# Performance work log

Measured on AMD Instinct MI355X. Metric: run time of the kernel, lower is better.

The kernel has to match this reference:

```python
import jax, jax.numpy as jnp
import numpy as np

SECURE_MIN = 1e-5
EPS = 1e-20
N_ITER = 10

def _l1_normalize(t, axis):
    # F.normalize(p=1): t / max(||t||_1, eps); t is nonnegative here so |t| = t
    n = jnp.sum(jnp.abs(t), axis=axis, keepdims=True)
    return t / jnp.maximum(n, EPS)

def setup_inputs() -> dict:
    key = jax.random.key(0)
    kx, kw = jax.random.split(key)
    B, F_in, F_out = 2048, 4096, 2048
    x = jax.random.uniform(kx, (B, F_in), dtype=jnp.float32)
    W = jax.random.uniform(kw, (F_out, F_in), dtype=jnp.float32)
    return {"x": x, "W": W}

def reference(x, W):
    B = x.shape[0]
    F_out = W.shape[0]
    # normalize_weights: clamp to secure min, L1-normalize each row (over input dim)
    Wn = _l1_normalize(jnp.clip(W, SECURE_MIN), axis=1)  # (F_out, F_in)
    # _prepare_input: L1 normalize over feature dim
    xn = _l1_normalize(x, axis=-1)  # (B, F_in)
    # _reset_h: uniform h over output units
    h0 = jnp.full((B, F_out), 1.0 / F_out, dtype=x.dtype)

    def step(h, _):
        # _reconstruct: h @ W -> input space
        recon = h @ Wn                                   # (B, F_in)
        recon = jnp.clip(recon, SECURE_MIN)              # _secure_tensor
        recon = _l1_normalize(recon, axis=-1)            # normalize_reconstruction
        update = (xn / recon) @ Wn.T                     # _forward, (B, F_out)
        h = h * update                                   # multiplicative NNMF update
        h = _l1_normalize(jnp.clip(h, SECURE_MIN), axis=-1)  # _process_h
        return h, None

    h, _ = jax.lax.scan(step, h0, None, length=N_ITER)
    return h
```

## Files before the change

kernel.cpp:

```cpp
#include <hip/hip_runtime.h>
#include <stdint.h>
#include <stddef.h>

#define B_DIM 2048
#define FIN   4096
#define FOUT  2048
#define NITER 10
#define SMIN  1e-5f

#define WSCALE 16384.0f
#define HSCALE 256.0f
#define OUTSCALE1 (1.0f / 4194304.0f)
#define RS_I8 56.0f

typedef float floatx16 __attribute__((ext_vector_type(16)));
typedef int   intx4    __attribute__((ext_vector_type(4)));
typedef int   intx8    __attribute__((ext_vector_type(8)));
typedef int   intx16   __attribute__((ext_vector_type(16)));

__device__ inline unsigned short f2bf(float f) {
    unsigned int u = __float_as_uint(f);
    u += 0x7fffu + ((u >> 16) & 1u);
    return (unsigned short)(u >> 16);
}
__device__ inline float bflo(unsigned int u) { return __uint_as_float(u << 16); }
__device__ inline float bfhi(unsigned int u) { return __uint_as_float(u & 0xffff0000u); }
__device__ inline unsigned int pack2(float a, float b) {
    return (unsigned int)f2bf(a) | ((unsigned int)f2bf(b) << 16);
}

__device__ inline void async16(const void* g, void* l) {
    __builtin_amdgcn_global_load_lds(
        (const __attribute__((address_space(1))) void*)g,
        (__attribute__((address_space(3))) void*)l, 16, 0, 0);
}

__device__ inline float block_row_sum(float v) {
    #pragma unroll
    for (int o = 32; o > 0; o >>= 1) v += __shfl_down(v, o, 64);
    __shared__ float red[4];
    const int lane = threadIdx.x & 63, w = threadIdx.x >> 6;
    if (lane == 0) red[w] = v;
    __syncthreads();
    return red[0] + red[1] + red[2] + red[3];
}

__device__ inline void block_sum_max(float s, float m, float* os, float* om) {
    #pragma unroll
    for (int o = 32; o > 0; o >>= 1) {
        s += __shfl_down(s, o, 64);
        m = fmaxf(m, __shfl_down(m, o, 64));
    }
    __shared__ float rs[4], rm[4];
    const int lane = threadIdx.x & 63, w = threadIdx.x >> 6;
    if (lane == 0) { rs[w] = s; rm[w] = m; }
    __syncthreads();
    *os = (rs[0] + rs[1]) + (rs[2] + rs[3]);
    *om = fmaxf(fmaxf(rm[0], rm[1]), fmaxf(rm[2], rm[3]));
}

__global__ __launch_bounds__(256) void k_norm_w(const float* __restrict__ W,
                                                unsigned char* __restrict__ Wn8,
                                                unsigned char* __restrict__ WnI8,
                                                float* __restrict__ dq) {
    const int row = blockIdx.x;
    const float4* src = (const float4*)(W + (size_t)row * FIN);
    float4 vals[4];
    float s = 0.f, m = 0.f;
    #pragma unroll
    for (int i = 0; i < 4; ++i) {
        float4 v = src[i * 256 + threadIdx.x];
        v.x = fmaxf(v.x, SMIN); v.y = fmaxf(v.y, SMIN);
        v.z = fmaxf(v.z, SMIN); v.w = fmaxf(v.w, SMIN);
        vals[i] = v;
        s += (v.x + v.y) + (v.z + v.w);
        m = fmaxf(m, fmaxf(fmaxf(v.x, v.y), fmaxf(v.z, v.w)));
    }
    block_sum_max(s, m, &s, &m);
    s = fmaxf(s, 1e-20f);
    const float inv8 = WSCALE / s;
    const float qi = 126.f / m;
    if (threadIdx.x == 0) dq[row] = m / (126.f * RS_I8 * s);
    unsigned int* d8 = (unsigned int*)(Wn8 + (size_t)row * FIN);
    unsigned int* di = (unsigned int*)(WnI8 + (size_t)row * FIN);
    #pragma unroll
    for (int i = 0; i < 4; ++i) {
        float4 v = vals[i];
        unsigned int u = 0;
        u = (unsigned int)__builtin_amdgcn_cvt_pk_fp8_f32(v.x * inv8, v.y * inv8, (int)u, false);
        u = (unsigned int)__builtin_amdgcn_cvt_pk_fp8_f32(v.z * inv8, v.w * inv8, (int)u, true);
        d8[i * 256 + threadIdx.x] = u;
        const int b0 = (int)(v.x * qi + 0.5f);
        const int b1 = (int)(v.y * qi + 0.5f);
        const int b2 = (int)(v.z * qi + 0.5f);
        const int b3 = (int)(v.w * qi + 0.5f);
        di[i * 256 + threadIdx.x] =
            (unsigned int)b0 | ((unsigned int)b1 << 8) |
            ((unsigned int)b2 << 16) | ((unsigned int)b3 << 24);
    }
}

__global__ __launch_bounds__(256) void k_norm_x(const float* __restrict__ x,
                                                unsigned int* __restrict__ xnb) {
    const int row = blockIdx.x;
    const float4* src = (const float4*)(x + (size_t)row * FIN);
    float4 vals[4];
    float s = 0.f;
    #pragma unroll
    for (int j = 0; j < 2; ++j) {
        const int idx = j * 256 + threadIdx.x;
        float4 a = src[2 * idx], b = src[2 * idx + 1];
        vals[2 * j] = a; vals[2 * j + 1] = b;
        s += (fabsf(a.x) + fabsf(a.y)) + (fabsf(a.z) + fabsf(a.w));
        s += (fabsf(b.x) + fabsf(b.y)) + (fabsf(b.z) + fabsf(b.w));
    }
    s = block_row_sum(s);
    const float inv = 1.f / fmaxf(s, 1e-20f);
    uint4* dst = (uint4*)(xnb + (size_t)row * (FIN / 2));
    #pragma unroll
    for (int j = 0; j < 2; ++j) {
        float4 a = vals[2 * j], b = vals[2 * j + 1];
        uint4 o;
        o.x = pack2(a.x * inv, a.y * inv);
        o.y = pack2(a.z * inv, a.w * inv);
        o.z = pack2(b.x * inv, b.y * inv);
        o.w = pack2(b.z * inv, b.w * inv);
        dst[j * 256 + threadIdx.x] = o;
    }
}

__global__ __launch_bounds__(256) void k_transpose_fp8(const unsigned char* __restrict__ src,
                                                       unsigned char* __restrict__ dst) {
    __shared__ unsigned char tile[32][33];
    const int bi = blockIdx.x * 32, bo = blockIdx.y * 32;
    const int tx = threadIdx.x, ty = threadIdx.y;
    #pragma unroll
    for (int j = 0; j < 4; ++j)
        tile[ty + j * 8][tx] = src[(size_t)(bo + ty + j * 8) * FIN + bi + tx];
    __syncthreads();
    #pragma unroll
    for (int j = 0; j < 4; ++j)
        dst[(size_t)(bi + ty + j * 8) * FOUT + bo + tx] = tile[tx][ty + j * 8];
}

__global__ __launch_bounds__(256) void k_init_h(float* __restrict__ h,
                                                unsigned int* __restrict__ h8u) {
    const int i = blockIdx.x * blockDim.x + threadIdx.x;
    const float hv = 1.f / (float)FOUT;
    float4 v; v.x = hv; v.y = hv; v.z = hv; v.w = hv;
    ((float4*)h)[i] = v;
    h8u[i] = 0x20202020u;
}

__global__ __launch_bounds__(256) void k_gemm_fp8(const unsigned char* __restrict__ A,
                                                  const unsigned char* __restrict__ Bm,
                                                  unsigned short* __restrict__ C,
                                                  int N, int K) {
    __shared__ __align__(16) unsigned char As[128 * 64];
    __shared__ __align__(16) unsigned char Bs[128 * 64];
    const int tid  = threadIdx.x;
    const int wave = tid >> 6;
    const int lane = tid & 63;

    const int id = blockIdx.y * 32 + blockIdx.x;
    const int j8 = id & 7, s = id >> 3;
    const int bm = ((j8 >> 2) * 8 + (s >> 3)) * 128;
    const int bn = ((j8 & 3) * 8 + (s & 7)) * 128;

    const int wr = (wave >> 1) * 64;
    const int wc = (wave & 1) * 64;
    const int l31 = lane & 31;
    const int half = lane >> 5;

    floatx16 acc[2][2] = {};

    const int lr = lane >> 2;
    const int ks = ((lane & 3) ^ ((lane >> 3) & 3)) * 16;
    const unsigned char* ga = A  + (size_t)(bm + wave * 32 + lr) * K + ks;
    const unsigned char* gb = Bm + (size_t)(bn + wave * 32 + lr) * K + ks;

    for (int k0 = 0; k0 < K; k0 += 64) {
        __syncthreads();
        #pragma unroll
        for (int j = 0; j < 2; ++j) {
            async16(ga + (size_t)j * 16 * K + k0, &As[wave * 2048 + j * 1024]);
            async16(gb + (size_t)j * 16 * K + k0, &Bs[wave * 2048 + j * 1024]);
        }
        __syncthreads();

        const int sw = (l31 >> 1) & 3;
        const int c0 = (((half << 1) | 0) ^ sw) << 4;
        const int c1 = (((half << 1) | 1) ^ sw) << 4;
        intx8 af[2], bf[2];
        #pragma unroll
        for (int t = 0; t < 2; ++t) {
            const int ra = (wr + t * 32 + l31) * 64;
            const int rb = (wc + t * 32 + l31) * 64;
            intx4 a0 = *(const intx4*)&As[ra + c0];
            intx4 a1 = *(const intx4*)&As[ra + c1];
            intx4 b0 = *(const intx4*)&Bs[rb + c0];
            intx4 b1 = *(const intx4*)&Bs[rb + c1];
            af[t] = (intx8){a0.x, a0.y, a0.z, a0.w, a1.x, a1.y, a1.z, a1.w};
            bf[t] = (intx8){b0.x, b0.y, b0.z, b0.w, b1.x, b1.y, b1.z, b1.w};
        }
        #pragma unroll
        for (int mt = 0; mt < 2; ++mt)
            #pragma unroll
            for (int nt = 0; nt < 2; ++nt)
                acc[mt][nt] = __builtin_amdgcn_mfma_scale_f32_32x32x64_f8f6f4(
                    af[mt], bf[nt], acc[mt][nt],
                    0, 0, 0, 0x7F7F7F7Fu, 0, 0x7F7F7F7Fu);
    }

    const int row0 = 4 * half;
    #pragma unroll
    for (int mt = 0; mt < 2; ++mt) {
        #pragma unroll
        for (int nt = 0; nt < 2; ++nt) {
            #pragma unroll
            for (int reg = 0; reg < 16; ++reg) {
                const int rr = bm + wr + mt * 32 + row0 + (reg & 3) + 8 * (reg >> 2);
                const int cc = bn + wc + nt * 32 + l31;
                C[(size_t)rr * N + cc] = f2bf(acc[mt][nt][reg] * OUTSCALE1);
            }
        }
    }
}

__global__ __launch_bounds__(256) void k_gemm_i8(const unsigned char* __restrict__ A,
                                                 const unsigned char* __restrict__ Bm,
                                                 const float* __restrict__ dq,
                                                 float* __restrict__ C,
                                                 int N, int K, int Ksub) {
    __shared__ __align__(16) unsigned char As[128 * 64];
    __shared__ __align__(16) unsigned char Bs[128 * 64];
    const int tid  = threadIdx.x;
    const int wave = tid >> 6;
    const int lane = tid & 63;

    const int id = blockIdx.y * 16 + blockIdx.x;
    const int j8 = id & 7, s = id >> 3;
    const int bm = ((j8 >> 1) * 4 + (s >> 3)) * 128;
    const int bn = ((j8 & 1) * 8 + (s & 7)) * 128;

    const int kz = blockIdx.z * Ksub;
    const int wr = (wave >> 1) * 64;
    const int wc = (wave & 1) * 64;
    const int l31 = lane & 31;
    const int half = lane >> 5;

    intx16 acc[2][2] = {};

    const int lr = lane >> 2;
    const int ks = ((lane & 3) ^ ((lane >> 3) & 3)) * 16;
    const unsigned char* ga = A  + (size_t)(bm + wave * 32 + lr) * K + ks;
    const unsigned char* gb = Bm + (size_t)(bn + wave * 32 + lr) * K + ks;

    for (int k0 = kz; k0 < kz + Ksub; k0 += 64) {
        __syncthreads();
        #pragma unroll
        for (int j = 0; j < 2; ++j) {
            async16(ga + (size_t)j * 16 * K + k0, &As[wave * 2048 + j * 1024]);
            async16(gb + (size_t)j * 16 * K + k0, &Bs[wave * 2048 + j * 1024]);
        }
        __syncthreads();

        const int sw = (l31 >> 1) & 3;
        #pragma unroll
        for (int kk = 0; kk < 2; ++kk) {
            const int slot = (((kk << 1) + half) ^ sw) << 4;
            intx4 af[2], bf[2];
            #pragma unroll
            for (int t = 0; t < 2; ++t) {
                af[t] = *(const intx4*)&As[(wr + t * 32 + l31) * 64 + slot];
                bf[t] = *(const intx4*)&Bs[(wc + t * 32 + l31) * 64 + slot];
            }
            #pragma unroll
            for (int mt = 0; mt < 2; ++mt)
                #pragma unroll
                for (int nt = 0; nt < 2; ++nt)
                    acc[mt][nt] = __builtin_amdgcn_mfma_i32_32x32x32_i8(
                        af[mt], bf[nt], acc[mt][nt], 0, 0, 0);
        }
    }

    float* Cz = C + (size_t)blockIdx.z * B_DIM * N;
    const int row0 = 4 * half;
    const float d0 = dq[bn + wc + l31];
    const float d1 = dq[bn + wc + 32 + l31];
    #pragma unroll
    for (int mt = 0; mt < 2; ++mt) {
        #pragma unroll
        for (int nt = 0; nt < 2; ++nt) {
            const float d = nt ? d1 : d0;
            #pragma unroll
            for (int reg = 0; reg < 16; ++reg) {
                const int rr = bm + wr + mt * 32 + row0 + (reg & 3) + 8 * (reg >> 2);
                const int cc = bn + wc + nt * 32 + l31;
                Cz[(size_t)rr * N + cc] = (float)acc[mt][nt][reg] * d;
            }
        }
    }
}

__global__ __launch_bounds__(256) void k_make_ratio(const unsigned short* __restrict__ rec,
                                                    const unsigned int* __restrict__ xnb,
                                                    unsigned char* __restrict__ ri8) {
    const int row = blockIdx.x;
    float v[16];
    float s = 0.f;
    #pragma unroll
    for (int g = 0; g < 2; ++g) {
        const int idx = g * 256 + threadIdx.x;
        uint4 u = ((const uint4*)(rec + (size_t)row * FIN))[idx];
        float* p = v + g * 8;
        p[0] = bflo(u.x); p[1] = bfhi(u.x); p[2] = bflo(u.y); p[3] = bfhi(u.y);
        p[4] = bflo(u.z); p[5] = bfhi(u.z); p[6] = bflo(u.w); p[7] = bfhi(u.w);
        #pragma unroll
        for (int e = 0; e < 8; ++e) { p[e] = fmaxf(p[e], SMIN); s += p[e]; }
    }
    s = block_row_sum(s);
    const float ss = s * RS_I8;
    #pragma unroll
    for (int g = 0; g < 2; ++g) {
        const int idx = g * 256 + threadIdx.x;
        uint4 xu = ((const uint4*)(xnb + (size_t)row * (FIN / 2)))[idx];
        float* p = v + g * 8;
        float r[8];
        r[0] = bflo(xu.x) * ss / p[0]; r[1] = bfhi(xu.x) * ss / p[1];
        r[2] = bflo(xu.y) * ss / p[2]; r[3] = bfhi(xu.y) * ss / p[3];
        r[4] = bflo(xu.z) * ss / p[4]; r[5] = bfhi(xu.z) * ss / p[5];
        r[6] = bflo(xu.w) * ss / p[6]; r[7] = bfhi(xu.w) * ss / p[7];
        unsigned int q[8];
        #pragma unroll
        for (int e = 0; e < 8; ++e)
            q[e] = (unsigned int)(int)(fminf(r[e], 127.0f) + 0.5f);
        uint2 o;
        o.x = q[0] | (q[1] << 8) | (q[2] << 16) | (q[3] << 24);
        o.y = q[4] | (q[5] << 8) | (q[6] << 16) | (q[7] << 24);
        ((uint2*)(ri8 + (size_t)row * FIN))[idx] = o;
    }
}

__global__ __launch_bounds__(256) void k_update_h(const float* __restrict__ hin,
                                                  const float* __restrict__ upd,
                                                  int nparts,
                                                  float* __restrict__ hout,
                                                  unsigned int* __restrict__ h8u) {
    const int row = blockIdx.x;
    const float4* hp = (const float4*)(hin + (size_t)row * FOUT);
    float4 vals[2];
    float s = 0.f;
    #pragma unroll
    for (int i = 0; i < 2; ++i) {
        const int idx = i * 256 + threadIdx.x;
        float4 hv = hp[idx];
        float4 uv = ((const float4*)(upd + (size_t)row * FOUT))[idx];
        for (int z = 1; z < nparts; ++z) {
            float4 p = ((const float4*)(upd + (size_t)z * B_DIM * FOUT + (size_t)row * FOUT))[idx];
            uv.x += p.x; uv.y += p.y; uv.z += p.z; uv.w += p.w;
        }
        float4 v;
        v.x = fmaxf(hv.x * uv.x, SMIN);
        v.y = fmaxf(hv.y * uv.y, SMIN);
        v.z = fmaxf(hv.z * uv.z, SMIN);
        v.w = fmaxf(hv.w * uv.w, SMIN);
        vals[i] = v;
        s += (v.x + v.y) + (v.z + v.w);
    }
    s = block_row_sum(s);
    const float inv = 1.f / fmaxf(s, 1e-20f);
    float4* op = (float4*)(hout + (size_t)row * FOUT);
    unsigned int* bp = h8u + (size_t)row * (FOUT / 4);
    #pragma unroll
    for (int i = 0; i < 2; ++i) {
        float4 v = vals[i];
        v.x *= inv; v.y *= inv; v.z *= inv; v.w *= inv;
        op[i * 256 + threadIdx.x] = v;
        unsigned int u = 0;
        u = (unsigned int)__builtin_amdgcn_cvt_pk_fp8_f32(v.x * HSCALE, v.y * HSCALE, (int)u, false);
        u = (unsigned int)__builtin_amdgcn_cvt_pk_fp8_f32(v.z * HSCALE, v.w * HSCALE, (int)u, true);
        bp[i * 256 + threadIdx.x] = u;
    }
}

extern "C" void kernel_launch(void* const* d_in, const int* in_sizes, int n_in,
                              void* d_out, int out_size, void* d_ws, size_t ws_size,
                              hipStream_t stream) {
    const float* x = (const float*)d_in[0];
    const float* W = (const float*)d_in[1];
    float* out = (float*)d_out;

    const size_t UPD_PART = (size_t)B_DIM * FOUT * 4;
    const size_t FIXED    = 81000000;
    int S2 = 1;
    if (ws_size >= FIXED + 2 * UPD_PART + (1 << 20)) {
        S2 = 2;
    }

    char* ws = (char*)d_ws;
    size_t off = 0;
    auto alloc = [&](size_t bytes) {
        void* p = ws + off;
        off += (bytes + 255) & ~(size_t)255;
        return p;
    };
    unsigned char*  WnT8 = (unsigned char*)alloc((size_t)FIN * FOUT);
    unsigned char*  WnI8 = (unsigned char*)alloc((size_t)FOUT * FIN);
    float*          dq   = (float*)alloc((size_t)FOUT * 4);
    unsigned int*   h8u  = (unsigned int*)alloc((size_t)B_DIM * FOUT);
    unsigned char*  ri8  = (unsigned char*)alloc((size_t)B_DIM * FIN);
    unsigned int*   xnb  = (unsigned int*)alloc((size_t)B_DIM * FIN * 2);
    float* h             = (float*)alloc((size_t)B_DIM * FOUT * 4);
    unsigned short* rec  = (unsigned short*)alloc((size_t)B_DIM * FIN * 2);
    float* upd           = (float*)alloc(UPD_PART * S2);
    unsigned char* Wn8 = (unsigned char*)rec;
    (void)in_sizes; (void)n_in; (void)out_size;

    k_norm_w<<<FOUT, 256, 0, stream>>>(W, Wn8, WnI8, dq);
    k_transpose_fp8<<<dim3(FIN / 32, FOUT / 32), dim3(32, 8), 0, stream>>>(Wn8, WnT8);
    k_norm_x<<<B_DIM, 256, 0, stream>>>(x, xnb);
    k_init_h<<<(B_DIM * FOUT) / (256 * 4), 256, 0, stream>>>(h, h8u);

    for (int it = 0; it < NITER; ++it) {
        k_gemm_fp8<<<dim3(FIN / 128, B_DIM / 128, 1), 256, 0, stream>>>(
            (const unsigned char*)h8u, WnT8, rec, FIN, FOUT);
        k_make_ratio<<<B_DIM, 256, 0, stream>>>(rec, xnb, ri8);
        k_gemm_i8<<<dim3(FOUT / 128, B_DIM / 128, S2), 256, 0, stream>>>(
            ri8, WnI8, dq, upd, FOUT, FIN, FIN / S2);
        k_update_h<<<B_DIM, 256, 0, stream>>>(h, upd, S2, (it == NITER - 1) ? out : h, h8u);
    }
}
```

Measured before the change: 846.8 us.

## Double-buffer LDS tiles in fp8 and int8 GEMM kernels

Both GEMM kernels now keep two LDS buffers for the A and B tiles. The async global-to-LDS copy for the next K slice is issued right after the barrier, so it runs while the MFMAs work on the current slice. This drops one of the two barriers per K step and hides load latency behind compute. In exchange, LDS per block doubles to 32 KB, which may reduce how many blocks fit on a CU.

After: 867.5 us. +2.4%, slower.

```diff
diff --git a/kernel.cpp b/kernel.cpp
--- a/kernel.cpp
+++ b/kernel.cpp
@@ -156,8 +156,8 @@
                                                   const unsigned char* __restrict__ Bm,
                                                   unsigned short* __restrict__ C,
                                                   int N, int K) {
-    __shared__ __align__(16) unsigned char As[128 * 64];
-    __shared__ __align__(16) unsigned char Bs[128 * 64];
+    __shared__ __align__(16) unsigned char As[2][128 * 64];
+    __shared__ __align__(16) unsigned char Bs[2][128 * 64];
     const int tid  = threadIdx.x;
     const int wave = tid >> 6;
     const int lane = tid & 63;
@@ -179,49 +179,56 @@
     const unsigned char* ga = A  + (size_t)(bm + wave * 32 + lr) * K + ks;
     const unsigned char* gb = Bm + (size_t)(bn + wave * 32 + lr) * K + ks;
 
-    for (int k0 = 0; k0 < K; k0 += 64) {
+    auto stage = [&](int k0, int buf) {
+        #pragma unroll
+        for (int j = 0; j < 2; ++j) {
+            async16(ga + (size_t)j * 16 * K + k0, &As[buf][wave * 2048 + j * 1024]);
+            async16(gb + (size_t)j * 16 * K + k0, &Bs[buf][wave * 2048 + j * 1024]);
+        }
+    };
+
+    const int nt = K >> 6;
+    stage(0, 0);
+    int cur = 0;
+    for (int t = 0; t < nt; ++t) {
         __syncthreads();
-        #pragma unroll
-        for (int j = 0; j < 2; ++j) {
-            async16(ga + (size_t)j * 16 * K + k0, &As[wave * 2048 + j * 1024]);
-            async16(gb + (size_t)j * 16 * K + k0, &Bs[wave * 2048 + j * 1024]);
-        }
-        __syncthreads();
+        if (t + 1 < nt) stage((t + 1) << 6, cur ^ 1);
 
         const int sw = (l31 >> 1) & 3;
         const int c0 = (((half << 1) | 0) ^ sw) << 4;
         const int c1 = (((half << 1) | 1) ^ sw) << 4;
         intx8 af[2], bf[2];
         #pragma unroll
-        for (int t = 0; t < 2; ++t) {
-            const int ra = (wr + t * 32 + l31) * 64;
-            const int rb = (wc + t * 32 + l31) * 64;
-            intx4 a0 = *(const intx4*)&As[ra + c0];
-            intx4 a1 = *(const intx4*)&As[ra + c1];
-            intx4 b0 = *(const intx4*)&Bs[rb + c0];
-            intx4 b1 = *(const intx4*)&Bs[rb + c1];
-            af[t] = (intx8){a0.x, a0.y, a0.z, a0.w, a1.x, a1.y, a1.z, a1.w};
-            bf[t] = (intx8){b0.x, b0.y, b0.z, b0.w, b1.x, b1.y, b1.z, b1.w};
+        for (int tt = 0; tt < 2; ++tt) {
+            const int ra = (wr + tt * 32 + l31) * 64;
+            const int rb = (wc + tt * 32 + l31) * 64;
+            intx4 a0 = *(const intx4*)&As[cur][ra + c0];
+            intx4 a1 = *(const intx4*)&As[cur][ra + c1];
+            intx4 b0 = *(const intx4*)&Bs[cur][rb + c0];
+            intx4 b1 = *(const intx4*)&Bs[cur][rb + c1];
+            af[tt] = (intx8){a0.x, a0.y, a0.z, a0.w, a1.x, a1.y, a1.z, a1.w};
+            bf[tt] = (intx8){b0.x, b0.y, b0.z, b0.w, b1.x, b1.y, b1.z, b1.w};
         }
         #pragma unroll
         for (int mt = 0; mt < 2; ++mt)
             #pragma unroll
-            for (int nt = 0; nt < 2; ++nt)
-                acc[mt][nt] = __builtin_amdgcn_mfma_scale_f32_32x32x64_f8f6f4(
-                    af[mt], bf[nt], acc[mt][nt],
+            for (int nt2 = 0; nt2 < 2; ++nt2)
+                acc[mt][nt2] = __builtin_amdgcn_mfma_scale_f32_32x32x64_f8f6f4(
+                    af[mt], bf[nt2], acc[mt][nt2],
                     0, 0, 0, 0x7F7F7F7Fu, 0, 0x7F7F7F7Fu);
+        cur ^= 1;
     }
 
     const int row0 = 4 * half;
     #pragma unroll
     for (int mt = 0; mt < 2; ++mt) {
         #pragma unroll
-        for (int nt = 0; nt < 2; ++nt) {
+        for (int nt2 = 0; nt2 < 2; ++nt2) {
             #pragma unroll
             for (int reg = 0; reg < 16; ++reg) {
                 const int rr = bm + wr + mt * 32 + row0 + (reg & 3) + 8 * (reg >> 2);
-                const int cc = bn + wc + nt * 32 + l31;
-                C[(size_t)rr * N + cc] = f2bf(acc[mt][nt][reg] * OUTSCALE1);
+                const int cc = bn + wc + nt2 * 32 + l31;
+                C[(size_t)rr * N + cc] = f2bf(acc[mt][nt2][reg] * OUTSCALE1);
             }
         }
     }
@@ -232,8 +239,8 @@
                                                  const float* __restrict__ dq,
                                                  float* __restrict__ C,
                                                  int N, int K, int Ksub) {
-    __shared__ __align__(16) unsigned char As[128 * 64];
-    __shared__ __align__(16) unsigned char Bs[128 * 64];
+    __shared__ __align__(16) unsigned char As[2][128 * 64];
+    __shared__ __align__(16) unsigned char Bs[2][128 * 64];
     const int tid  = threadIdx.x;
     const int wave = tid >> 6;
     const int lane = tid & 63;
@@ -256,14 +263,20 @@
     const unsigned char* ga = A  + (size_t)(bm + wave * 32 + lr) * K + ks;
     const unsigned char* gb = Bm + (size_t)(bn + wave * 32 + lr) * K + ks;
 
-    for (int k0 = kz; k0 < kz + Ksub; k0 += 64) {
+    auto stage = [&](int k0, int buf) {
+        #pragma unroll
+        for (int j = 0; j < 2; ++j) {
+            async16(ga + (size_t)j * 16 * K + k0, &As[buf][wave * 2048 + j * 1024]);
+            async16(gb + (size_t)j * 16 * K + k0, &Bs[buf][wave * 2048 + j * 1024]);
+        }
+    };
+
+    const int nt = Ksub >> 6;
+    stage(kz, 0);
+    int cur = 0;
+    for (int t = 0; t < nt; ++t) {
         __syncthreads();
-        #pragma unroll
-        for (int j = 0; j < 2; ++j) {
-            async16(ga + (size_t)j * 16 * K + k0, &As[wave * 2048 + j * 1024]);
-            async16(gb + (size_t)j * 16 * K + k0, &Bs[wave * 2048 + j * 1024]);
-        }
-        __syncthreads();
+        if (t + 1 < nt) stage(kz + ((t + 1) << 6), cur ^ 1);
 
         const int sw = (l31 >> 1) & 3;
         #pragma unroll
@@ -271,17 +284,18 @@
             const int slot = (((kk << 1) + half) ^ sw) << 4;
             intx4 af[2], bf[2];
             #pragma unroll
-            for (int t = 0; t < 2; ++t) {
-                af[t] = *(const intx4*)&As[(wr + t * 32 + l31) * 64 + slot];
-                bf[t] = *(const intx4*)&Bs[(wc + t * 32 + l31) * 64 + slot];
+            for (int tt = 0; tt < 2; ++tt) {
+                af[tt] = *(const intx4*)&As[cur][(wr + tt * 32 + l31) * 64 + slot];
+                bf[tt] = *(const intx4*)&Bs[cur][(wc + tt * 32 + l31) * 64 + slot];
             }
             #pragma unroll
             for (int mt = 0; mt < 2; ++mt)
                 #pragma unroll
-                for (int nt = 0; nt < 2; ++nt)
-                    acc[mt][nt] = __builtin_amdgcn_mfma_i32_32x32x32_i8(
-                        af[mt], bf[nt], acc[mt][nt], 0, 0, 0);
-        }
+                for (int nt2 = 0; nt2 < 2; ++nt2)
+                    acc[mt][nt2] = __builtin_amdgcn_mfma_i32_32x32x32_i8(
+                        af[mt], bf[nt2], acc[mt][nt2], 0, 0, 0);
+        }
+        cur ^= 1;
     }
 
     float* Cz = C + (size_t)blockIdx.z * B_DIM * N;
@@ -291,13 +305,13 @@
     #pragma unroll
     for (int mt = 0; mt < 2; ++mt) {
         #pragma unroll
-        for (int nt = 0; nt < 2; ++nt) {
-            const float d = nt ? d1 : d0;
+        for (int nt2 = 0; nt2 < 2; ++nt2) {
+            const float d = nt2 ? d1 : d0;
             #pragma unroll
             for (int reg = 0; reg < 16; ++reg) {
                 const int rr = bm + wr + mt * 32 + row0 + (reg & 3) + 8 * (reg >> 2);
-                const int cc = bn + wc + nt * 32 + l31;
-                Cz[(size_t)rr * N + cc] = (float)acc[mt][nt][reg] * d;
+                const int cc = bn + wc + nt2 * 32 + l31;
+                Cz[(size_t)rr * N + cc] = (float)acc[mt][nt2][reg] * d;
             }
         }
     }
```
